# Kernel tuning notes

Measured on AMD Instinct MI355X. Metric: run time of the kernel, lower is better.

## Reference

```python
import jax, jax.numpy as jnp
import numpy as np

N_NODES = 100000
N_EDGES = 3200000
D_IN = 512
D_OUT = 512


def setup_inputs() -> dict:
    key = jax.random.key(0)
    k1, k2, k3, k4, k5 = jax.random.split(key, 5)
    features = jax.random.normal(k1, (N_NODES, D_IN), dtype=jnp.float32)
    edge_src = jax.random.randint(k2, (N_EDGES,), 0, N_NODES, dtype=jnp.int32)
    edge_dst = jnp.sort(jax.random.randint(k3, (N_EDGES,), 0, N_NODES, dtype=jnp.int32))
    # normalized-adjacency-like positive edge weights
    edge_weight = jax.random.uniform(k4, (N_EDGES,), dtype=jnp.float32)
    # xavier_uniform_ for weight [D_IN, D_OUT]
    limit = float(np.sqrt(6.0 / (D_IN + D_OUT)))
    weight = jax.random.uniform(k5, (D_IN, D_OUT), dtype=jnp.float32,
                                minval=-limit, maxval=limit)
    return {
        "features": features,
        "weight": weight,
        "edge_src": edge_src,
        "edge_dst": edge_dst,
        "edge_weight": edge_weight,
        "times": 3,
    }


def reference(features, weight, edge_src, edge_dst, edge_weight, times):
    n_nodes = features.shape[0]
    # dense feature transform: support = features @ W
    support = features @ weight  # [N, D_OUT]

    def spmm(x):
        # out[dst] += w * x[src]  (one hop of sparse adjacency propagation)
        msgs = x[edge_src] * edge_weight[:, None]  # [E, D_OUT]
        return jax.ops.segment_sum(msgs, edge_dst, num_segments=n_nodes)

    output = spmm(support)
    for _ in range(times - 1):
        output = spmm(output)
    return output
```

## Files before the change

kernel.cpp:

```cpp
#include <hip/hip_runtime.h>

#define N_NODES_C 100000
#define N_EDGES_C 3200000
#define DDIM 512

typedef float v4f __attribute__((ext_vector_type(4)));
typedef unsigned int v4u __attribute__((ext_vector_type(4)));
typedef unsigned short v4h __attribute__((ext_vector_type(4)));
typedef _Float16 v8hf __attribute__((ext_vector_type(8)));

__device__ inline unsigned short f2h(float f) {
    union { _Float16 h; unsigned short u; } v;
    v.h = (_Float16)f;
    return v.u;
}
__device__ inline float h2f(unsigned short s) {
    union { unsigned short u; _Float16 h; } v;
    v.u = s;
    return (float)v.h;
}

__global__ __launch_bounds__(256) void build_rowptr(const int* __restrict__ dst,
                                                    int* __restrict__ rp) {
    int n = blockIdx.x * blockDim.x + threadIdx.x;
    if (n > N_NODES_C) return;
    int lo = 0, hi = N_EDGES_C;
    while (lo < hi) {
        int mid = (lo + hi) >> 1;
        if (dst[mid] < n) lo = mid + 1;
        else hi = mid;
    }
    rp[n] = lo;
}

__global__ __launch_bounds__(256) void gemm_f16(const float* __restrict__ A,
                                                const float* __restrict__ B,
                                                unsigned short* __restrict__ C,
                                                int M) {
    __shared__ unsigned short sA[128][40];
    __shared__ unsigned short sBt[128][40];

    const int tid  = threadIdx.x;
    const int lane = tid & 63;
    const int wave = tid >> 6;
    const int quad = lane >> 4;
    const int l16  = lane & 15;
    const int wr   = (wave >> 1) * 64;
    const int wc   = (wave & 1) * 64;
    const int m0   = blockIdx.x * 128;
    const int n0   = blockIdx.y * 128;

    const int ar = tid >> 3;
    const int ak = (tid & 7) * 4;
    const int bk = tid >> 5;
    const int bc = (tid & 31) * 4;

    v4f acc[4][4] = {};

    for (int k0 = 0; k0 < DDIM; k0 += 32) {
#pragma unroll
        for (int rr = 0; rr < 4; ++rr) {
            const int row = ar + rr * 32;
            const int gm  = m0 + row;
            v4f a4 = {0.f, 0.f, 0.f, 0.f};
            if (gm < M) a4 = *(const v4f*)&A[(size_t)gm * DDIM + k0 + ak];
            v4h h;
            h.x = f2h(a4.x); h.y = f2h(a4.y); h.z = f2h(a4.z); h.w = f2h(a4.w);
            *(v4h*)&sA[row][ak] = h;
        }
#pragma unroll
        for (int kr = 0; kr < 4; ++kr) {
            const int k = bk + kr * 8;
            v4f b4 = *(const v4f*)&B[(size_t)(k0 + k) * DDIM + n0 + bc];
            sBt[bc + 0][k] = f2h(b4.x);
            sBt[bc + 1][k] = f2h(b4.y);
            sBt[bc + 2][k] = f2h(b4.z);
            sBt[bc + 3][k] = f2h(b4.w);
        }
        __syncthreads();

        v8hf af[4], bf[4];
#pragma unroll
        for (int i = 0; i < 4; ++i)
            af[i] = *(const v8hf*)&sA[wr + i * 16 + l16][quad * 8];
#pragma unroll
        for (int j = 0; j < 4; ++j)
            bf[j] = *(const v8hf*)&sBt[wc + j * 16 + l16][quad * 8];
#pragma unroll
        for (int i = 0; i < 4; ++i)
#pragma unroll
            for (int j = 0; j < 4; ++j)
                acc[i][j] = __builtin_amdgcn_mfma_f32_16x16x32_f16(
                    af[i], bf[j], acc[i][j], 0, 0, 0);
        __syncthreads();
    }

#pragma unroll
    for (int i = 0; i < 4; ++i) {
#pragma unroll
        for (int j = 0; j < 4; ++j) {
#pragma unroll
            for (int r = 0; r < 4; ++r) {
                const int rg = m0 + wr + i * 16 + quad * 4 + r;
                const int cg = n0 + wc + j * 16 + l16;
                if (rg < M) C[(size_t)rg * DDIM + cg] = f2h(acc[i][j][r]);
            }
        }
    }
}

__device__ inline void fma8(float* acc, float w, v4u v) {
#pragma unroll
    for (int q = 0; q < 4; ++q) {
        const unsigned int u = v[q];
        acc[2 * q]     = fmaf(w, h2f((unsigned short)(u & 0xffffu)), acc[2 * q]);
        acc[2 * q + 1] = fmaf(w, h2f((unsigned short)(u >> 16)),     acc[2 * q + 1]);
    }
}

template <bool OUT_F32>
__global__ __launch_bounds__(256) void spmm_f16(const v4u* __restrict__ x,
                                                const int* __restrict__ esrc,
                                                const float* __restrict__ ew,
                                                const int* __restrict__ rp,
                                                void* __restrict__ y) {
    const int wave = threadIdx.x >> 6;
    const int lane = threadIdx.x & 63;
    const int n = blockIdx.x * 4 + wave;
    const int s = rp[n];
    const int e = rp[n + 1];

    float a0[8] = {}, a1[8] = {}, a2[8] = {}, a3[8] = {};

    int i = s;
    for (; i + 3 < e; i += 4) {
        const int s0 = esrc[i];
        const int s1 = esrc[i + 1];
        const int s2 = esrc[i + 2];
        const int s3 = esrc[i + 3];
        const float w0 = ew[i];
        const float w1 = ew[i + 1];
        const float w2 = ew[i + 2];
        const float w3 = ew[i + 3];
        v4u v0 = x[(size_t)s0 * 64 + lane];
        v4u v1 = x[(size_t)s1 * 64 + lane];
        v4u v2 = x[(size_t)s2 * 64 + lane];
        v4u v3 = x[(size_t)s3 * 64 + lane];
        fma8(a0, w0, v0);
        fma8(a1, w1, v1);
        fma8(a2, w2, v2);
        fma8(a3, w3, v3);
    }
    for (; i < e; ++i) {
        const int sI = esrc[i];
        const float wI = ew[i];
        v4u vI = x[(size_t)sI * 64 + lane];
        fma8(a0, wI, vI);
    }

    float r[8];
#pragma unroll
    for (int q = 0; q < 8; ++q) r[q] = (a0[q] + a1[q]) + (a2[q] + a3[q]);

    if (OUT_F32) {
        float* yo = (float*)y;
        v4f o0 = {r[0], r[1], r[2], r[3]};
        v4f o1 = {r[4], r[5], r[6], r[7]};
        *(v4f*)&yo[(size_t)n * DDIM + lane * 8] = o0;
        *(v4f*)&yo[(size_t)n * DDIM + lane * 8 + 4] = o1;
    } else {
        v4u o;
        o.x = (unsigned int)f2h(r[0]) | ((unsigned int)f2h(r[1]) << 16);
        o.y = (unsigned int)f2h(r[2]) | ((unsigned int)f2h(r[3]) << 16);
        o.z = (unsigned int)f2h(r[4]) | ((unsigned int)f2h(r[5]) << 16);
        o.w = (unsigned int)f2h(r[6]) | ((unsigned int)f2h(r[7]) << 16);
        ((v4u*)y)[(size_t)n * 64 + lane] = o;
    }
}

extern "C" void kernel_launch(void* const* d_in, const int* in_sizes, int n_in,
                              void* d_out, int out_size, void* d_ws, size_t ws_size,
                              hipStream_t stream) {
    const float* features = (const float*)d_in[0];
    const float* weight   = (const float*)d_in[1];
    const int*   esrc     = (const int*)d_in[2];
    const int*   edst     = (const int*)d_in[3];
    const float* ew       = (const float*)d_in[4];

    float* out = (float*)d_out;
    char*  ws  = (char*)d_ws;

    int* rp = (int*)ws;
    size_t rp_bytes = ((size_t)(N_NODES_C + 1) * sizeof(int) + 511) & ~(size_t)511;
    unsigned short* S = (unsigned short*)(ws + rp_bytes);
    unsigned short* Y = S + (size_t)N_NODES_C * DDIM;

    build_rowptr<<<(N_NODES_C + 256) / 256, 256, 0, stream>>>(edst, rp);

    dim3 ggrid((N_NODES_C + 127) / 128, DDIM / 128);
    gemm_f16<<<ggrid, 256, 0, stream>>>(features, weight, S, N_NODES_C);

    const int sgrid = N_NODES_C / 4;
    spmm_f16<false><<<sgrid, 256, 0, stream>>>((const v4u*)S, esrc, ew, rp, Y);
    spmm_f16<false><<<sgrid, 256, 0, stream>>>((const v4u*)Y, esrc, ew, rp, S);
    spmm_f16<true ><<<sgrid, 256, 0, stream>>>((const v4u*)S, esrc, ew, rp, out);
}
```

Baseline: 1.905 ms.

## Pre-convert features to fp16, load GEMM A tiles via global_load_lds, deepen SpMM unroll

Adds a separate kernel that converts the features to fp16 once, so the GEMM can stream its A tiles straight into LDS with direct global-to-LDS loads instead of converting in registers. The SpMM kernel now keeps its row bounds in scalar registers, gathers 8 edges per iteration instead of 4 to keep more loads in flight, and writes the final fp32 output with nontemporal stores. The extra conversion pass adds a full read of the fp32 features and a write of an fp16 copy, which offsets part of the GEMM saving. The GEMM accounts for only a small share of the total time, which is dominated by the gathers.

```diff
diff --git a/kernel.cpp b/kernel.cpp
--- a/kernel.cpp
+++ b/kernel.cpp
@@ -18,6 +18,13 @@
     union { unsigned short u; _Float16 h; } v;
     v.u = s;
     return (float)v.h;
+}
+
+__device__ __forceinline__ void gload_lds16(const void* g, void* l) {
+    __builtin_amdgcn_global_load_lds(
+        (const __attribute__((address_space(1))) unsigned int*)(void*)(g),
+        (__attribute__((address_space(3))) unsigned int*)(l),
+        16, 0, 0);
 }
 
 __global__ __launch_bounds__(256) void build_rowptr(const int* __restrict__ dst,
@@ -33,11 +40,24 @@
     rp[n] = lo;
 }
 
-__global__ __launch_bounds__(256) void gemm_f16(const float* __restrict__ A,
-                                                const float* __restrict__ B,
-                                                unsigned short* __restrict__ C,
-                                                int M) {
-    __shared__ unsigned short sA[128][40];
+__global__ __launch_bounds__(256) void convert_x(const v4f* __restrict__ X,
+                                                 v4u* __restrict__ Xh) {
+    const size_t i = (size_t)blockIdx.x * 256 + threadIdx.x;
+    const v4f a = X[2 * i];
+    const v4f b = X[2 * i + 1];
+    v4u o;
+    o.x = (unsigned)f2h(a.x) | ((unsigned)f2h(a.y) << 16);
+    o.y = (unsigned)f2h(a.z) | ((unsigned)f2h(a.w) << 16);
+    o.z = (unsigned)f2h(b.x) | ((unsigned)f2h(b.y) << 16);
+    o.w = (unsigned)f2h(b.z) | ((unsigned)f2h(b.w) << 16);
+    Xh[i] = o;
+}
+
+__global__ __launch_bounds__(256) void gemm2(const unsigned short* __restrict__ Ah,
+                                             const float* __restrict__ B,
+                                             unsigned short* __restrict__ C,
+                                             int M) {
+    __shared__ unsigned short sA[128 * 32];
     __shared__ unsigned short sBt[128][40];
 
     const int tid  = threadIdx.x;
@@ -50,24 +70,23 @@
     const int m0   = blockIdx.x * 128;
     const int n0   = blockIdx.y * 128;
 
-    const int ar = tid >> 3;
-    const int ak = (tid & 7) * 4;
+    int ar0 = m0 + (tid >> 2);
+    int ar1 = ar0 + 64;
+    if (ar0 >= M) ar0 = 0;
+    if (ar1 >= M) ar1 = 0;
+    const unsigned short* ga0 = Ah + (size_t)ar0 * DDIM + (tid & 3) * 8;
+    const unsigned short* ga1 = Ah + (size_t)ar1 * DDIM + (tid & 3) * 8;
+    unsigned short* la0 = &sA[wave * 512];
+    unsigned short* la1 = &sA[2048 + wave * 512];
+
     const int bk = tid >> 5;
     const int bc = (tid & 31) * 4;
 
     v4f acc[4][4] = {};
 
     for (int k0 = 0; k0 < DDIM; k0 += 32) {
-#pragma unroll
-        for (int rr = 0; rr < 4; ++rr) {
-            const int row = ar + rr * 32;
-            const int gm  = m0 + row;
-            v4f a4 = {0.f, 0.f, 0.f, 0.f};
-            if (gm < M) a4 = *(const v4f*)&A[(size_t)gm * DDIM + k0 + ak];
-            v4h h;
-            h.x = f2h(a4.x); h.y = f2h(a4.y); h.z = f2h(a4.z); h.w = f2h(a4.w);
-            *(v4h*)&sA[row][ak] = h;
-        }
+        gload_lds16(ga0 + k0, la0);
+        gload_lds16(ga1 + k0, la1);
 #pragma unroll
         for (int kr = 0; kr < 4; ++kr) {
             const int k = bk + kr * 8;
@@ -82,7 +101,7 @@
         v8hf af[4], bf[4];
 #pragma unroll
         for (int i = 0; i < 4; ++i)
-            af[i] = *(const v8hf*)&sA[wr + i * 16 + l16][quad * 8];
+            af[i] = *(const v8hf*)&sA[(wr + i * 16 + l16) * 32 + quad * 8];
 #pragma unroll
         for (int j = 0; j < 4; ++j)
             bf[j] = *(const v8hf*)&sBt[wc + j * 16 + l16][quad * 8];
@@ -119,21 +138,55 @@
 }
 
 template <bool OUT_F32>
-__global__ __launch_bounds__(256) void spmm_f16(const v4u* __restrict__ x,
-                                                const int* __restrict__ esrc,
-                                                const float* __restrict__ ew,
-                                                const int* __restrict__ rp,
-                                                void* __restrict__ y) {
+__global__ __launch_bounds__(256) void spmm2(const v4u* __restrict__ x,
+                                             const int* __restrict__ esrc,
+                                             const float* __restrict__ ew,
+                                             const int* __restrict__ rp,
+                                             void* __restrict__ y) {
     const int wave = threadIdx.x >> 6;
     const int lane = threadIdx.x & 63;
-    const int n = blockIdx.x * 4 + wave;
-    const int s = rp[n];
-    const int e = rp[n + 1];
+    const int n = __builtin_amdgcn_readfirstlane(blockIdx.x * 4 + wave);
+    const int s = __builtin_amdgcn_readfirstlane(rp[n]);
+    const int e = __builtin_amdgcn_readfirstlane(rp[n + 1]);
 
     float a0[8] = {}, a1[8] = {}, a2[8] = {}, a3[8] = {};
 
     int i = s;
-    for (; i + 3 < e; i += 4) {
+    for (; i + 7 < e; i += 8) {
+        const int s0 = esrc[i];
+        const int s1 = esrc[i + 1];
+        const int s2 = esrc[i + 2];
+        const int s3 = esrc[i + 3];
+        const int s4 = esrc[i + 4];
+        const int s5 = esrc[i + 5];
+        const int s6 = esrc[i + 6];
+        const int s7 = esrc[i + 7];
+        const float w0 = ew[i];
+        const float w1 = ew[i + 1];
+        const float w2 = ew[i + 2];
+        const float w3 = ew[i + 3];
+        const float w4 = ew[i + 4];
+        const float w5 = ew[i + 5];
+        const float w6 = ew[i + 6];
+        const float w7 = ew[i + 7];
+        v4u v0 = x[(size_t)s0 * 64 + lane];
+        v4u v1 = x[(size_t)s1 * 64 + lane];
+        v4u v2 = x[(size_t)s2 * 64 + lane];
+        v4u v3 = x[(size_t)s3 * 64 + lane];
+        v4u v4 = x[(size_t)s4 * 64 + lane];
+        v4u v5 = x[(size_t)s5 * 64 + lane];
+        v4u v6 = x[(size_t)s6 * 64 + lane];
+        v4u v7 = x[(size_t)s7 * 64 + lane];
+        fma8(a0, w0, v0);
+        fma8(a1, w1, v1);
+        fma8(a2, w2, v2);
+        fma8(a3, w3, v3);
+        fma8(a0, w4, v4);
+        fma8(a1, w5, v5);
+        fma8(a2, w6, v6);
+        fma8(a3, w7, v7);
+    }
+    if (i + 3 < e) {
         const int s0 = esrc[i];
         const int s1 = esrc[i + 1];
         const int s2 = esrc[i + 2];
@@ -150,6 +203,7 @@
         fma8(a1, w1, v1);
         fma8(a2, w2, v2);
         fma8(a3, w3, v3);
+        i += 4;
     }
     for (; i < e; ++i) {
         const int sI = esrc[i];
@@ -166,8 +220,8 @@
         float* yo = (float*)y;
         v4f o0 = {r[0], r[1], r[2], r[3]};
         v4f o1 = {r[4], r[5], r[6], r[7]};
-        *(v4f*)&yo[(size_t)n * DDIM + lane * 8] = o0;
-        *(v4f*)&yo[(size_t)n * DDIM + lane * 8 + 4] = o1;
+        __builtin_nontemporal_store(o0, (v4f*)&yo[(size_t)n * DDIM + lane * 8]);
+        __builtin_nontemporal_store(o1, (v4f*)&yo[(size_t)n * DDIM + lane * 8 + 4]);
     } else {
         v4u o;
         o.x = (unsigned int)f2h(r[0]) | ((unsigned int)f2h(r[1]) << 16);
@@ -194,14 +248,18 @@
     size_t rp_bytes = ((size_t)(N_NODES_C + 1) * sizeof(int) + 511) & ~(size_t)511;
     unsigned short* S = (unsigned short*)(ws + rp_bytes);
     unsigned short* Y = S + (size_t)N_NODES_C * DDIM;
+    unsigned short* Xh = Y;
 
     build_rowptr<<<(N_NODES_C + 256) / 256, 256, 0, stream>>>(edst, rp);
 
+    convert_x<<<(N_NODES_C * DDIM / 8) / 256, 256, 0, stream>>>(
+        (const v4f*)features, (v4u*)Xh);
+
     dim3 ggrid((N_NODES_C + 127) / 128, DDIM / 128);
-    gemm_f16<<<ggrid, 256, 0, stream>>>(features, weight, S, N_NODES_C);
+    gemm2<<<ggrid, 256, 0, stream>>>(Xh, weight, S, N_NODES_C);
 
     const int sgrid = N_NODES_C / 4;
-    spmm_f16<false><<<sgrid, 256, 0, stream>>>((const v4u*)S, esrc, ew, rp, Y);
-    spmm_f16<false><<<sgrid, 256, 0, stream>>>((const v4u*)Y, esrc, ew, rp, S);
-    spmm_f16<true ><<<sgrid, 256, 0, stream>>>((const v4u*)S, esrc, ew, rp, out);
-}
+    spmm2<false><<<sgrid, 256, 0, stream>>>((const v4u*)S, esrc, ew, rp, Y);
+    spmm2<false><<<sgrid, 256, 0, stream>>>((const v4u*)Y, esrc, ew, rp, S);
+    spmm2<true ><<<sgrid, 256, 0, stream>>>((const v4u*)S, esrc, ew, rp, out);
+}
```

New measurement: 1.962 ms. 3.0% more time.
